# Kernel tuning notes

Measured on AMD Instinct MI355X. Metric: run time of the kernel, lower is better.

Reference implementation:

```python
import math
import jax, jax.numpy as jnp
import numpy as np

B, T, D, H = 1, 4096, 1024, 16
HD = D // H  # 64

def setup_inputs() -> dict:
    key = jax.random.key(0)
    k1, k2, k3 = jax.random.split(key, 3)
    x = jax.random.normal(k1, (B, T, D), dtype=jnp.float32)
    # torch nn.Linear weight layout: [out_features, in_features]
    w_attn = jax.random.normal(k2, (3 * D, D), dtype=jnp.float32) * (1.0 / math.sqrt(D))
    w_proj = jax.random.normal(k3, (D, D), dtype=jnp.float32) * (1.0 / math.sqrt(D))
    return {"x": x, "w_attn": w_attn, "w_proj": w_proj}

def reference(x, w_attn, w_proj):
    b, t, d = x.shape
    qkv = jnp.einsum('btd,ed->bte', x, w_attn)  # [B,T,3D]
    q, k, v = jnp.split(qkv, 3, axis=-1)
    # [B,H,T,HD]
    q = q.reshape(b, t, H, HD).transpose(0, 2, 1, 3)
    k = k.reshape(b, t, H, HD).transpose(0, 2, 1, 3)
    v = v.reshape(b, t, H, HD).transpose(0, 2, 1, 3)
    scale = 1.0 / math.sqrt(HD)
    att = jnp.einsum('bhqd,bhkd->bhqk', q, k) * scale  # [B,H,T,T]
    causal = jnp.tril(jnp.ones((t, t), dtype=bool))
    att = jnp.where(causal[None, None], att, -jnp.inf)
    att = jax.nn.softmax(att, axis=-1)
    y = jnp.einsum('bhqk,bhkd->bhqd', att, v)  # [B,H,T,HD]
    y = y.transpose(0, 2, 1, 3).reshape(b, t, d)
    return jnp.einsum('btd,ed->bte', y, w_proj)
```

## Files before the change

kernel.cpp:

```cpp
#include <hip/hip_runtime.h>
#include <hip/hip_bf16.h>

typedef __bf16 bf16x8 __attribute__((ext_vector_type(8)));
typedef float  f32x4  __attribute__((ext_vector_type(4)));
typedef short  sh4    __attribute__((ext_vector_type(4)));

__device__ __forceinline__ void async_load16(const void* g, void* l) {
    __builtin_amdgcn_global_load_lds(
        (const __attribute__((address_space(1))) unsigned int*)g,
        (__attribute__((address_space(3))) unsigned int*)l,
        16, 0, 0);
}

__device__ __forceinline__ bool sniff_is_bf16(const void* src) {
    const unsigned int* p = (const unsigned int*)src;
    unsigned v = p[threadIdx.x & 63];
    unsigned e = (v >> 7) & 0xFF;
    unsigned long long m = __ballot(e >= 100 && e <= 140);
    return __popcll(m) >= 48;
}

__global__ __launch_bounds__(256) void to_bf16(const void* __restrict__ src,
                                               __bf16* __restrict__ dst, int n) {
    bool b16 = sniff_is_bf16(src);
    int i = (blockIdx.x * 256 + threadIdx.x) * 4;
    if (i >= n) return;
    if (b16) {
        *(uint2*)(dst + i) = *(const uint2*)((const __bf16*)src + i);
    } else {
        float4 v = *(const float4*)((const float*)src + i);
        dst[i]     = (__bf16)v.x;
        dst[i + 1] = (__bf16)v.y;
        dst[i + 2] = (__bf16)v.z;
        dst[i + 3] = (__bf16)v.w;
    }
}

__global__ __launch_bounds__(256) void gemm_bt(
    const __bf16* __restrict__ A,
    const __bf16* __restrict__ B,
    void* __restrict__ Cv,
    int M, int N, int K,
    const void* sniff)
{
    bool out_b16 = true;
    if (sniff) out_b16 = sniff_is_bf16(sniff);

    __shared__ __bf16 As[128 * 32];
    __shared__ __bf16 Bs[128 * 32];

    const int nwg = gridDim.x;
    const int cpx = nwg >> 3;
    const int sid = (blockIdx.x & 7) * cpx + (blockIdx.x >> 3);
    const int nbx = N >> 7;
    const int bx  = sid % nbx;
    const int by  = sid / nbx;

    const int tid  = threadIdx.x;
    const int lane = tid & 63;
    const int w    = tid >> 6;
    const int wm   = w >> 1, wn = w & 1;
    const int m0   = by * 128;
    const int n0   = bx * 128;
    const int c    = lane & 15;
    const int g    = lane >> 4;

    f32x4 acc[4][4] = {};

    const int e0 = tid * 8;
    const int e1 = e0 + 2048;
    const int r0 = e0 >> 5, c0 = e0 & 31;
    const int r1 = e1 >> 5, c1 = e1 & 31;

    for (int k0 = 0; k0 < K; k0 += 32) {
        async_load16(A + (size_t)(m0 + r0) * K + k0 + c0, As + e0);
        async_load16(A + (size_t)(m0 + r1) * K + k0 + c1, As + e1);
        async_load16(B + (size_t)(n0 + r0) * K + k0 + c0, Bs + e0);
        async_load16(B + (size_t)(n0 + r1) * K + k0 + c1, Bs + e1);
        __syncthreads();

        bf16x8 af[4], bfr[4];
        #pragma unroll
        for (int i = 0; i < 4; i++)
            af[i] = *(const bf16x8*)&As[(wm * 64 + i * 16 + c) * 32 + g * 8];
        #pragma unroll
        for (int j = 0; j < 4; j++)
            bfr[j] = *(const bf16x8*)&Bs[(wn * 64 + j * 16 + c) * 32 + g * 8];
        #pragma unroll
        for (int i = 0; i < 4; i++)
            #pragma unroll
            for (int j = 0; j < 4; j++)
                acc[i][j] = __builtin_amdgcn_mfma_f32_16x16x32_bf16(af[i], bfr[j], acc[i][j], 0, 0, 0);
        __syncthreads();
    }

    #pragma unroll
    for (int i = 0; i < 4; i++) {
        const int row0 = m0 + wm * 64 + i * 16 + g * 4;
        #pragma unroll
        for (int j = 0; j < 4; j++) {
            const int col = n0 + wn * 64 + j * 16 + c;
            #pragma unroll
            for (int r = 0; r < 4; r++) {
                const size_t idx = (size_t)(row0 + r) * N + col;
                if (out_b16) ((__bf16*)Cv)[idx] = (__bf16)acc[i][j][r];
                else         ((float*)Cv)[idx]  = acc[i][j][r];
            }
        }
    }
}

__global__ __launch_bounds__(256) void vtrans(const __bf16* __restrict__ qkv,
                                              __bf16* __restrict__ vT) {
    __shared__ __bf16 Lt[64 * 72];
    const int tid = threadIdx.x;
    const int h   = blockIdx.y;
    const int t0  = blockIdx.x * 64;
    #pragma unroll
    for (int rr = 0; rr < 2; rr++) {
        int e = rr * 2048 + tid * 8;
        int tr = e >> 6, tc = e & 63;
        bf16x8 v = *(const bf16x8*)&qkv[(size_t)(t0 + tr) * 3072 + 2048 + h * 64 + tc];
        #pragma unroll
        for (int i = 0; i < 8; i++) Lt[(tc + i) * 72 + tr] = v[i];
    }
    __syncthreads();
    #pragma unroll
    for (int rr = 0; rr < 2; rr++) {
        int e = rr * 2048 + tid * 8;
        int dr = e >> 6, dc = e & 63;
        *(bf16x8*)&vT[(size_t)h * 262144 + (size_t)dr * 4096 + t0 + dc]
            = *(const bf16x8*)&Lt[dr * 72 + dc];
    }
}

__global__ __launch_bounds__(512, 4) void attn_fwd(
    const __bf16* __restrict__ qkv,
    const __bf16* __restrict__ vT,
    __bf16* __restrict__ y)
{
    constexpr int LDQ = 3072;
    constexpr float SCL = 0.18033688011112042f;
    constexpr float MEXP = 16.0f;

    __shared__ __align__(16) char raw[50176];
    __bf16* ksb = (__bf16*)raw;
    __bf16* vsb = (__bf16*)(raw + 24576);
    float*  ls  = (float*)(raw + 49152);
    float*  F   = (float*)raw;

    const int id   = blockIdx.x;
    const int h    = (id & 7) * 2 + (id >> 8);
    const int pr   = (id >> 3) & 31;
    const int tid  = threadIdx.x;
    const int lane = tid & 63;
    const int w    = tid >> 6;
    const int kw   = w & 3;
    const int qw   = w >> 2;
    const int c    = lane & 15;
    const int g    = lane >> 4;
    const int qoff = h * 64;

    const int sr = tid >> 3, sg = ((tid & 7) ^ (sr & 7)) * 8;
    const __bf16* vbase = vT + (size_t)h * 262144;

    const int qts[2] = {63 - pr, pr};

    #pragma unroll 1
    for (int ph = 0; ph < 2; ph++) {
        const int qt  = qts[ph];
        const int qs  = qt * 64;
        const int nkt = qt + 1;

        __syncthreads();

        async_load16(qkv + (size_t)sr * LDQ + 1024 + qoff + sg, ksb + tid * 8);
        async_load16(vbase + (size_t)sr * 4096 + sg, vsb + tid * 8);
        if (nkt > 1) {
            async_load16(qkv + (size_t)(64 + sr) * LDQ + 1024 + qoff + sg, ksb + 4096 + tid * 8);
            async_load16(vbase + (size_t)sr * 4096 + 64 + sg, vsb + 4096 + tid * 8);
        }

        bf16x8 qf[2][2];
        #pragma unroll
        for (int n = 0; n < 2; n++) {
            const __bf16* qrow = qkv + (size_t)(qs + qw * 32 + n * 16 + c) * LDQ + qoff;
            bf16x8 q0 = *(const bf16x8*)(qrow + g * 8);
            bf16x8 q1 = *(const bf16x8*)(qrow + 32 + g * 8);
            #pragma unroll
            for (int i = 0; i < 8; i++) {
                qf[n][0][i] = (__bf16)((float)q0[i] * SCL);
                qf[n][1][i] = (__bf16)((float)q1[i] * SCL);
            }
        }

        float l_lane[2] = {};
        f32x4 o[4][2] = {};

        for (int t = 0; t < nkt; t++) {
            if (t + 1 < nkt) asm volatile("s_waitcnt vmcnt(2)" ::: "memory");
            else             asm volatile("s_waitcnt vmcnt(0)" ::: "memory");
            __builtin_amdgcn_s_barrier();
            asm volatile("" ::: "memory");

            if (t + 2 < nkt) {
                const int nks = (t + 2) * 64;
                const int nb  = (t + 2) % 3;
                async_load16(qkv + (size_t)(nks + sr) * LDQ + 1024 + qoff + sg, ksb + (nb * 4096 + tid * 8));
                async_load16(vbase + (size_t)sr * 4096 + nks + sg, vsb + (nb * 4096 + tid * 8));
            }

            const __bf16* ks_ = ksb + (t % 3) * 4096;
            const __bf16* vs_ = vsb + (t % 3) * 4096;

            f32x4 sa[2] = {};
            #pragma unroll
            for (int s = 0; s < 2; s++) {
                bf16x8 kf = *(const bf16x8*)&ks_[(kw * 16 + c) * 64 + ((s * 4 + g) ^ (c & 7)) * 8];
                #pragma unroll
                for (int n = 0; n < 2; n++)
                    sa[n] = __builtin_amdgcn_mfma_f32_16x16x32_bf16(kf, qf[n][s], sa[n], 0, 0, 0);
            }

            if (t == nkt - 1) {
                #pragma unroll
                for (int n = 0; n < 2; n++)
                    #pragma unroll
                    for (int r = 0; r < 4; r++)
                        if (kw * 16 + g * 4 + r > qw * 32 + n * 16 + c) sa[n][r] = -1e30f;
            }

            sh4 vf[4];
            #pragma unroll
            for (int j = 0; j < 4; j++)
                vf[j] = *(const sh4*)&vs_[(j * 16 + c) * 64 + ((2 * kw + (g >> 1)) ^ (c & 7)) * 8 + (g & 1) * 4];

            #pragma unroll
            for (int n = 0; n < 2; n++) {
                __bf16 pb[4] __attribute__((aligned(8)));
                #pragma unroll
                for (int r = 0; r < 4; r++) {
                    float p = __builtin_amdgcn_exp2f(sa[n][r] - MEXP);
                    l_lane[n] += p;
                    pb[r] = (__bf16)p;
                }
                sh4 pbs = *(const sh4*)pb;
                #pragma unroll
                for (int j = 0; j < 4; j++)
                    o[j][n] = __builtin_amdgcn_mfma_f32_16x16x16bf16_1k(vf[j], pbs, o[j][n], 0, 0, 0);
            }
        }

        #pragma unroll
        for (int n = 0; n < 2; n++) {
            l_lane[n] += __shfl_xor(l_lane[n], 16);
            l_lane[n] += __shfl_xor(l_lane[n], 32);
        }
        __syncthreads();
        if (g == 0) {
            #pragma unroll
            for (int n = 0; n < 2; n++) ls[(kw * 4 + qw * 2 + n) * 16 + c] = l_lane[n];
        }
        __syncthreads();
        float rl = 0.f;
        if (w < 4) {
            float l_run = ls[(0 * 4 + w) * 16 + c] + ls[(1 * 4 + w) * 16 + c]
                        + ls[(2 * 4 + w) * 16 + c] + ls[(3 * 4 + w) * 16 + c];
            rl = 1.0f / l_run;
        }

        #pragma unroll
        for (int j = 0; j < 4; j++) {
            __syncthreads();
            #pragma unroll
            for (int n = 0; n < 2; n++)
                *(f32x4*)&F[((kw * 64) + (qw * 32 + n * 16 + c)) * 20 + g * 4] = o[j][n];
            __syncthreads();
            if (w < 4) {
                f32x4 t0 = *(const f32x4*)&F[((0 * 64) + (w * 16 + c)) * 20 + g * 4];
                f32x4 t1 = *(const f32x4*)&F[((1 * 64) + (w * 16 + c)) * 20 + g * 4];
                f32x4 t2 = *(const f32x4*)&F[((2 * 64) + (w * 16 + c)) * 20 + g * 4];
                f32x4 t3 = *(const f32x4*)&F[((3 * 64) + (w * 16 + c)) * 20 + g * 4];
                f32x4 tt = t0 + t1 + t2 + t3;
                __bf16 ob[4] __attribute__((aligned(8)));
                #pragma unroll
                for (int r = 0; r < 4; r++) ob[r] = (__bf16)(tt[r] * rl);
                *(uint2*)&y[(size_t)(qs + w * 16 + c) * 1024 + qoff + j * 16 + g * 4]
                    = *(const uint2*)ob;
            }
        }
    }
}

extern "C" void kernel_launch(void* const* d_in, const int* in_sizes, int n_in,
                              void* d_out, int out_size, void* d_ws, size_t ws_size,
                              hipStream_t stream) {
    constexpr int T = 4096, D = 1024;

    __bf16* cx   = (__bf16*)d_ws;
    __bf16* cwa  = cx  + (size_t)T * D;
    __bf16* cwp  = cwa + (size_t)3 * D * D;
    __bf16* qkv  = cwp + (size_t)D * D;
    __bf16* y    = qkv + (size_t)T * 3 * D;
    __bf16* vT   = cx;

    to_bf16<<<T * D / 1024, 256, 0, stream>>>(d_in[0], cx, T * D);
    to_bf16<<<3 * D * D / 1024, 256, 0, stream>>>(d_in[1], cwa, 3 * D * D);
    to_bf16<<<D * D / 1024, 256, 0, stream>>>(d_in[2], cwp, D * D);

    gemm_bt<<<(3 * D / 128) * (T / 128), 256, 0, stream>>>(cx, cwa, qkv, T, 3 * D, D, nullptr);
    vtrans<<<dim3(T / 64, 16), 256, 0, stream>>>(qkv, vT);
    attn_fwd<<<512, 512, 0, stream>>>(qkv, vT, y);
    gemm_bt<<<(D / 128) * (T / 128), 256, 0, stream>>>(y, cwp, d_out, T, D, D, d_in[2]);
}
```

Before: 211.3 us.

## Triple-buffer GEMM LDS tiles with async prefetch two stages ahead

Replaces the single-buffered load-sync-compute-sync loop in gemm_bt with a three-stage LDS ring buffer. The tiles for iterations kt+1 and kt+2 are issued with async global-to-LDS loads, and each step waits with vmcnt and one barrier. This lets global memory latency overlap the MFMA work and removes one barrier per iteration. It triples the LDS footprint to 48KB, which may lower occupancy, and correctness depends on the hand-placed waitcnt counts.

```diff
diff --git a/kernel.cpp b/kernel.cpp
--- a/kernel.cpp
+++ b/kernel.cpp
@@ -46,8 +46,8 @@
     bool out_b16 = true;
     if (sniff) out_b16 = sniff_is_bf16(sniff);
 
-    __shared__ __bf16 As[128 * 32];
-    __shared__ __bf16 Bs[128 * 32];
+    __shared__ __bf16 As[3 * 128 * 32];
+    __shared__ __bf16 Bs[3 * 128 * 32];
 
     const int nwg = gridDim.x;
     const int cpx = nwg >> 3;
@@ -72,26 +72,55 @@
     const int r0 = e0 >> 5, c0 = e0 & 31;
     const int r1 = e1 >> 5, c1 = e1 & 31;
 
-    for (int k0 = 0; k0 < K; k0 += 32) {
-        async_load16(A + (size_t)(m0 + r0) * K + k0 + c0, As + e0);
-        async_load16(A + (size_t)(m0 + r1) * K + k0 + c1, As + e1);
-        async_load16(B + (size_t)(n0 + r0) * K + k0 + c0, Bs + e0);
-        async_load16(B + (size_t)(n0 + r1) * K + k0 + c1, Bs + e1);
-        __syncthreads();
+    const __bf16* a0 = A + (size_t)(m0 + r0) * K + c0;
+    const __bf16* a1 = A + (size_t)(m0 + r1) * K + c1;
+    const __bf16* b0 = B + (size_t)(n0 + r0) * K + c0;
+    const __bf16* b1 = B + (size_t)(n0 + r1) * K + c1;
+
+    const int KT = K >> 5;
+
+    async_load16(a0, As + e0);
+    async_load16(a1, As + e1);
+    async_load16(b0, Bs + e0);
+    async_load16(b1, Bs + e1);
+    async_load16(a0 + 32, As + 4096 + e0);
+    async_load16(a1 + 32, As + 4096 + e1);
+    async_load16(b0 + 32, Bs + 4096 + e0);
+    async_load16(b1 + 32, Bs + 4096 + e1);
+
+    int cb = 0, sb = 2;
+    for (int kt = 0; kt < KT; ++kt) {
+        if (kt + 1 < KT) asm volatile("s_waitcnt vmcnt(4)" ::: "memory");
+        else             asm volatile("s_waitcnt vmcnt(0)" ::: "memory");
+        __builtin_amdgcn_s_barrier();
+        asm volatile("" ::: "memory");
+
+        if (kt + 2 < KT) {
+            const int k0 = (kt + 2) << 5;
+            async_load16(a0 + k0, As + sb * 4096 + e0);
+            async_load16(a1 + k0, As + sb * 4096 + e1);
+            async_load16(b0 + k0, Bs + sb * 4096 + e0);
+            async_load16(b1 + k0, Bs + sb * 4096 + e1);
+        }
+
+        const __bf16* as_ = As + cb * 4096;
+        const __bf16* bs_ = Bs + cb * 4096;
 
         bf16x8 af[4], bfr[4];
         #pragma unroll
         for (int i = 0; i < 4; i++)
-            af[i] = *(const bf16x8*)&As[(wm * 64 + i * 16 + c) * 32 + g * 8];
+            af[i] = *(const bf16x8*)&as_[(wm * 64 + i * 16 + c) * 32 + g * 8];
         #pragma unroll
         for (int j = 0; j < 4; j++)
-            bfr[j] = *(const bf16x8*)&Bs[(wn * 64 + j * 16 + c) * 32 + g * 8];
+            bfr[j] = *(const bf16x8*)&bs_[(wn * 64 + j * 16 + c) * 32 + g * 8];
         #pragma unroll
         for (int i = 0; i < 4; i++)
             #pragma unroll
             for (int j = 0; j < 4; j++)
                 acc[i][j] = __builtin_amdgcn_mfma_f32_16x16x32_bf16(af[i], bfr[j], acc[i][j], 0, 0, 0);
-        __syncthreads();
+
+        cb = (cb == 2) ? 0 : cb + 1;
+        sb = (sb == 2) ? 0 : sb + 1;
     }
 
     #pragma unroll
```

After: 208.1 us. About the same (-1.5%).
